# Kernel optimization log

Hardware: AMD Instinct MI355X
Metric: run time of the kernel (lower is better)

The kernel has to match this reference:

```python
import jax, jax.numpy as jnp
import numpy as np

B, S, E, H, D, L, V, O = 64, 512, 512, 8, 64, 4, 50000, 1000
KW, STRIDE = 5, 5
L_OUT = (S - KW) // STRIDE + 1  # 102


def setup_inputs() -> dict:
    key = jax.random.key(0)
    ks = jax.random.split(key, 20)
    sc = 0.02
    inp = {
        'tokens': jax.random.randint(ks[0], (B, S), 0, V, dtype=jnp.int32),
        'emb': jax.random.normal(ks[1], (V + 1, E), jnp.float32) * sc,
        'Wq': jax.random.normal(ks[2], (L, H, E, D), jnp.float32) * sc,
        'bq': jnp.zeros((L, H, D), jnp.float32),
        'Wk': jax.random.normal(ks[3], (L, H, E, D), jnp.float32) * sc,
        'bk': jnp.zeros((L, H, D), jnp.float32),
        'Wv': jax.random.normal(ks[4], (L, H, E, D), jnp.float32) * sc,
        'bv': jnp.zeros((L, H, D), jnp.float32),
        'Wo': jax.random.normal(ks[5], (L, H * D, E), jnp.float32) * sc,
        'bo': jnp.zeros((L, E), jnp.float32),
        'W1': jax.random.normal(ks[6], (L, E, 2 * E), jnp.float32) * sc,
        'b1': jnp.zeros((L, 2 * E), jnp.float32),
        'W2': jax.random.normal(ks[7], (L, 2 * E, E), jnp.float32) * sc,
        'b2': jnp.zeros((L, E), jnp.float32),
        'Wc': jax.random.normal(ks[8], (KW, E, 1), jnp.float32) * sc,
        'bc': jnp.zeros((1,), jnp.float32),
        'Wd': jax.random.normal(ks[9], (L_OUT, O), jnp.float32) * sc,
        'bd': jnp.zeros((O,), jnp.float32),
    }
    return inp


def _l2_normalize(x, eps=1e-12):
    # tf.math.l2_normalize: x / sqrt(max(sum(x^2), eps))
    sq = jnp.sum(x * x, axis=-1, keepdims=True)
    return x * jax.lax.rsqrt(jnp.maximum(sq, eps))


def _forward(tokens, emb, Wq, bq, Wk, bk, Wv, bv, Wo, bo, W1, b1, W2, b2, Wc, bc, Wd, bd):
    mask = jnp.sign(tokens).astype(jnp.float32)[..., None]  # [B,S,1]
    out = emb[tokens] * mask                                 # [B,S,E]
    scale = 1.0 / jnp.sqrt(jnp.float32(E))                   # note: scaled by EMBEDDING_DIM, as in source
    for i in range(L):
        # per-head QKV projections, batched over heads
        q = jnp.einsum('bse,hed->bhsd', out, Wq[i]) + bq[i][None, :, None, :]
        k = jnp.einsum('bse,hed->bhsd', out, Wk[i]) + bk[i][None, :, None, :]
        v = jnp.einsum('bse,hed->bhsd', out, Wv[i]) + bv[i][None, :, None, :]
        scores = jnp.einsum('bhsd,bhtd->bhst', q, k) * scale
        attn = jax.nn.softmax(scores, axis=-1)
        heads = jnp.einsum('bhst,bhtd->bhsd', attn, v)       # [B,H,S,D]
        cat = heads.transpose(0, 2, 1, 3).reshape(B, S, H * D)
        mh = cat @ Wo[i] + bo[i]
        out = _l2_normalize(out + mh)
        ff = jax.nn.relu(out @ W1[i] + b1[i]) @ W2[i] + b2[i]
        out = ff + out
    # Conv1D(1, 5, strides=5) then squeeze channel, Dense over seq-length axis, softmax
    conv = jax.lax.conv_general_dilated(
        out, Wc, window_strides=(STRIDE,), padding='VALID',
        dimension_numbers=('NWC', 'WIO', 'NWC')) + bc          # [B,L_OUT,1]
    pooled = jnp.squeeze(conv, axis=-1)                        # [B,L_OUT]
    logits = pooled @ Wd + bd                                  # [B,O]
    return jax.nn.softmax(logits, axis=-1)


def reference(tokens, emb, Wq, bq, Wk, bk, Wv, bv, Wo, bo, W1, b1, W2, b2, Wc, bc, Wd, bd):
    return _forward(tokens, emb, Wq, bq, Wk, bk, Wv, bv, Wo, bo, W1, b1, W2, b2, Wc, bc, Wd, bd)
```

## Files before the change

### kernel.cpp

```cpp
#include <hip/hip_runtime.h>
#include <cstddef>

constexpr int B_ = 64, S_ = 512, E_ = 512, H_ = 8, D_ = 64, L_ = 4, O_ = 1000;
constexpr int BS_ = B_ * S_;
constexpr int HD_ = H_ * D_;
constexpr int QS_ = 1536;
constexpr int LOUT_ = 102;
constexpr float SCALE_ = 0.04419417382415922f;

typedef __bf16 bf16x8 __attribute__((ext_vector_type(8)));
typedef __bf16 bf16x4 __attribute__((ext_vector_type(4)));
typedef __bf16 bf16x2 __attribute__((ext_vector_type(2)));
typedef float floatx4 __attribute__((ext_vector_type(4)));

__device__ inline void load16_lds(const __bf16* g, __bf16* l) {
  __builtin_amdgcn_global_load_lds(
      (const __attribute__((address_space(1))) void*)g,
      (__attribute__((address_space(3))) void*)l, 16, 0, 0);
}

__global__ __launch_bounds__(256) void transpose_bf16(
    const float* __restrict__ in, __bf16* __restrict__ out,
    int R, int C, int IZ, int OZL, int OZH) {
  __shared__ float t[32][33];
  int z = blockIdx.z;
  const float* inz = in + (size_t)z * IZ;
  __bf16* outz = out + (size_t)(z >> 3) * OZL + (size_t)(z & 7) * OZH;
  int c0 = blockIdx.x * 32, r0 = blockIdx.y * 32;
  int x = threadIdx.x, y = threadIdx.y;
#pragma unroll
  for (int j = 0; j < 32; j += 8) t[y + j][x] = inz[(size_t)(r0 + y + j) * C + c0 + x];
  __syncthreads();
#pragma unroll
  for (int j = 0; j < 32; j += 8)
    outz[(size_t)(c0 + y + j) * R + r0 + x] = (__bf16)t[x][y + j];
}

__global__ __launch_bounds__(256) void bias_concat(
    const float* __restrict__ bq, const float* __restrict__ bk,
    const float* __restrict__ bv, float* __restrict__ qkvb) {
  int idx = blockIdx.x * 256 + threadIdx.x;
  int l = idx / QS_, j = idx % QS_;
  float v;
  if (j < 512) v = bq[l * 512 + j];
  else if (j < 1024) v = bk[l * 512 + j - 512];
  else v = bv[l * 512 + j - 1024];
  qkvb[idx] = v;
}

__global__ __launch_bounds__(256) void embed_kernel(
    const int* __restrict__ tokens, const float* __restrict__ emb,
    float* __restrict__ X, __bf16* __restrict__ Ab) {
  int idx = blockIdx.x * 256 + threadIdx.x;
  int bs = idx >> 7;
  int e = (idx & 127) << 2;
  int tok = tokens[bs];
  float4 v;
  if (tok == 0) v = make_float4(0.f, 0.f, 0.f, 0.f);
  else v = *(const float4*)(emb + (size_t)tok * E_ + e);
  size_t off = (size_t)bs * E_ + e;
  *(float4*)(X + off) = v;
  bf16x4 b;
  b[0] = (__bf16)v.x; b[1] = (__bf16)v.y; b[2] = (__bf16)v.z; b[3] = (__bf16)v.w;
  *(bf16x4*)(Ab + off) = b;
}

template <int RELU, int RES, int OUTF, int OUTB, int SCQ, int KT>
__global__ __launch_bounds__(256) void gemm_bf16(
    const __bf16* __restrict__ A, const __bf16* __restrict__ Bt,
    const float* __restrict__ bias, const float* __restrict__ Rsd,
    float* __restrict__ Cf, __bf16* __restrict__ Cb, int N, int lda, int Nt) {
  __shared__ __align__(16) __bf16 smem[24576];
  int tid = threadIdx.x;
  int lane = tid & 63, w = tid >> 6;
  int Mt8 = (int)(gridDim.x / Nt) >> 3;
  int xcd = blockIdx.x & 7;
  int j = blockIdx.x >> 3;
  int rr = j % (2 * Nt), chunk = j / (2 * Nt);
  int mt = xcd * Mt8 + chunk * 2 + (rr & 1);
  int nt = rr >> 1;
  int m0 = mt * 128, n0 = nt * 128;
  int q4 = lane >> 4, a_ = lane & 15;
  const int ldb = KT * 32;
  int r0s = tid >> 2, q0s = (tid & 3) ^ ((r0s >> 1) & 3);
  int r1s = 64 + (tid >> 2), q1s = (tid & 3) ^ ((r1s >> 1) & 3);
  const __bf16* Ag = A + (size_t)m0 * lda;
  const __bf16* Bg = Bt + (size_t)n0 * ldb;

  floatx4 acc[4][4];
#pragma unroll
  for (int i = 0; i < 4; ++i)
#pragma unroll
    for (int jj = 0; jj < 4; ++jj) acc[i][jj] = (floatx4)(0.0f);

  auto STAGE = [&](int kt, int bs) {
    __bf16* Ad = smem + bs * 4096;
    __bf16* Bd = smem + 12288 + bs * 4096;
    int k0 = kt * 32;
    load16_lds(Ag + (size_t)r0s * lda + k0 + q0s * 8, Ad + tid * 8);
    load16_lds(Ag + (size_t)r1s * lda + k0 + q1s * 8, Ad + (256 + tid) * 8);
    load16_lds(Bg + (size_t)r0s * ldb + k0 + q0s * 8, Bd + tid * 8);
    load16_lds(Bg + (size_t)r1s * ldb + k0 + q1s * 8, Bd + (256 + tid) * 8);
  };

  STAGE(0, 0);
  if (KT > 1) STAGE(1, 1);
#pragma unroll
  for (int kt = 0; kt < KT; ++kt) {
    if (kt + 2 < KT) {
      STAGE(kt + 2, (kt + 2) % 3);
      asm volatile("s_waitcnt vmcnt(8)" ::: "memory");
    } else if (kt + 1 < KT) {
      asm volatile("s_waitcnt vmcnt(4)" ::: "memory");
    } else {
      asm volatile("s_waitcnt vmcnt(0)" ::: "memory");
    }
    __builtin_amdgcn_s_barrier();
    __builtin_amdgcn_sched_barrier(0);
    const __bf16* As = smem + (kt % 3) * 4096;
    const __bf16* Bs = smem + 12288 + (kt % 3) * 4096;
    bf16x8 af[4], bfr[4];
#pragma unroll
    for (int i = 0; i < 4; ++i) {
      int row = (w & 1) * 64 + i * 16 + a_;
      int pc = q4 ^ ((row >> 1) & 3);
      af[i] = *(const bf16x8*)&As[(row * 4 + pc) * 8];
    }
#pragma unroll
    for (int jc = 0; jc < 4; ++jc) {
      int row = (w >> 1) * 64 + jc * 16 + a_;
      int pc = q4 ^ ((row >> 1) & 3);
      bfr[jc] = *(const bf16x8*)&Bs[(row * 4 + pc) * 8];
    }
    __builtin_amdgcn_s_setprio(1);
#pragma unroll
    for (int i = 0; i < 4; ++i)
#pragma unroll
      for (int jc = 0; jc < 4; ++jc)
        acc[i][jc] = __builtin_amdgcn_mfma_f32_16x16x32_bf16(bfr[jc], af[i],
                                                             acc[i][jc], 0, 0, 0);
    __builtin_amdgcn_s_setprio(0);
    asm volatile("" ::: "memory");
    __builtin_amdgcn_s_barrier();
  }
#pragma unroll
  for (int i = 0; i < 4; ++i) {
    int ml = (w & 1) * 64 + i * 16 + a_;
    int m = m0 + ml;
#pragma unroll
    for (int jc = 0; jc < 4; ++jc) {
      int nl = (w >> 1) * 64 + jc * 16 + q4 * 4;
      int n = n0 + nl;
      float4 bi = *(const float4*)(bias + n);
      floatx4 v = acc[i][jc];
      v[0] += bi.x; v[1] += bi.y; v[2] += bi.z; v[3] += bi.w;
      if (SCQ) { if (n < 512) v *= SCALE_; }
      if (RES) {
        float4 rv = *(const float4*)(Rsd + (size_t)m * N + n);
        v[0] += rv.x; v[1] += rv.y; v[2] += rv.z; v[3] += rv.w;
      }
      if (RELU) {
#pragma unroll
        for (int r = 0; r < 4; ++r) v[r] = fmaxf(v[r], 0.f);
      }
      if (OUTF) {
        float4 o = make_float4(v[0], v[1], v[2], v[3]);
        *(float4*)(Cf + (size_t)m * N + n) = o;
      }
      if (OUTB) {
        bf16x4 ob;
#pragma unroll
        for (int r = 0; r < 4; ++r) ob[r] = (__bf16)v[r];
        *(bf16x4*)&smem[ml * 136 + nl] = ob;
      }
    }
  }
  if (OUTB) {
    __syncthreads();
#pragma unroll
    for (int it = 0; it < 8; ++it) {
      int cid = it * 256 + tid;
      int row = cid >> 4, c8 = cid & 15;
      bf16x8 val = *(const bf16x8*)&smem[row * 136 + c8 * 8];
      *(bf16x8*)(Cb + (size_t)(m0 + row) * N + n0 + c8 * 8) = val;
    }
  }
}

__global__ __launch_bounds__(256, 2) void attn_bf16(__bf16* __restrict__ QKV) {
  __shared__ __align__(16) __bf16 Qs[256 * 64];
  __shared__ __align__(16) __bf16 Ks[64 * 64];
  __shared__ __align__(16) __bf16 Vt[64 * 64];
  __shared__ __align__(16) __bf16 Ps[64 * 64];
  int tid = threadIdx.x, lane = tid & 63, w = tid >> 6;
  int q4 = lane >> 4, a_ = lane & 15;
  int bid = blockIdx.x;
  int xg = bid & 7, slot = bid >> 3;
  int b = (slot >> 4) * 8 + xg;
  int r_ = slot & 15;
  int h = r_ >> 1;
  int s0 = (r_ & 1) * 256;
  size_t rowbase = (size_t)b * S_ * QS_ + h * 64;
  __bf16* Qg = QKV + rowbase;
  const __bf16* Kg = QKV + rowbase + 512;
  const __bf16* Vg = QKV + rowbase + 1024;
#pragma unroll
  for (int j = 0; j < 8; ++j) {
    int ci = j * 256 + w * 64 + lane;
    int row = ci >> 3, c = ci & 7, q = c ^ (row & 7);
    load16_lds(Qg + (size_t)(s0 + row) * QS_ + q * 8, Qs + (j * 256 + w * 64) * 8);
  }
  float mrow[4], lrow[4];
  floatx4 accO[4][4];
#pragma unroll
  for (int cc = 0; cc < 4; ++cc) {
    mrow[cc] = -3.0e38f; lrow[cc] = 0.f;
#pragma unroll
    for (int jc = 0; jc < 4; ++jc) accO[cc][jc] = (floatx4)(0.0f);
  }

  for (int t0 = 0; t0 < S_; t0 += 64) {
#pragma unroll
    for (int j = 0; j < 2; ++j) {
      int ci = j * 256 + w * 64 + lane;
      int row = ci >> 3, c = ci & 7, q = c ^ (row & 7);
      load16_lds(Kg + (size_t)(t0 + row) * QS_ + q * 8, Ks + (j * 256 + w * 64) * 8);
    }
    {
      int tp = tid & 31, dg = tid >> 5;
      bf16x8 v0 = *(const bf16x8*)(Vg + (size_t)(t0 + 2 * tp) * QS_ + dg * 8);
      bf16x8 v1 = *(const bf16x8*)(Vg + (size_t)(t0 + 2 * tp + 1) * QS_ + dg * 8);
#pragma unroll
      for (int x = 0; x < 8; ++x) {
        int d = dg * 8 + x;
        bf16x2 p; p[0] = v0[x]; p[1] = v1[x];
        *(bf16x2*)&Vt[(d * 8 + ((tp >> 2) ^ (d & 7))) * 8 + (tp & 3) * 2] = p;
      }
    }
    __syncthreads();
    bf16x8 af[2][4], bv[2][4];
#pragma unroll
    for (int ks = 0; ks < 2; ++ks)
#pragma unroll
      for (int jc = 0; jc < 4; ++jc) {
        int row = jc * 16 + a_, q = ks * 4 + q4;
        af[ks][jc] = *(const bf16x8*)&Ks[(row * 8 + (q ^ (row & 7))) * 8];
        bv[ks][jc] = *(const bf16x8*)&Vt[(row * 8 + (q ^ (row & 7))) * 8];
      }
#pragma unroll
    for (int cc = 0; cc < 4; ++cc) {
      int sbase = (cc * 4 + w) * 16;
      floatx4 sc[4];
#pragma unroll
      for (int jc = 0; jc < 4; ++jc) sc[jc] = (floatx4)(0.0f);
#pragma unroll
      for (int ks = 0; ks < 2; ++ks) {
        int row = sbase + a_, q = ks * 4 + q4;
        bf16x8 bq = *(const bf16x8*)&Qs[(row * 8 + (q ^ (row & 7))) * 8];
#pragma unroll
        for (int jc = 0; jc < 4; ++jc)
          sc[jc] = __builtin_amdgcn_mfma_f32_16x16x32_bf16(af[ks][jc], bq,
                                                           sc[jc], 0, 0, 0);
      }
      float mx = sc[0][0];
#pragma unroll
      for (int jc = 0; jc < 4; ++jc)
#pragma unroll
        for (int r = 0; r < 4; ++r) mx = fmaxf(mx, sc[jc][r]);
      mx = fmaxf(mx, __shfl_xor(mx, 16));
      mx = fmaxf(mx, __shfl_xor(mx, 32));
      float mnew = fmaxf(mrow[cc], mx);
      float alpha = __expf(mrow[cc] - mnew);
      mrow[cc] = mnew;
      float ps = 0.f;
      int prow = w * 16 + a_;
#pragma unroll
      for (int jc = 0; jc < 4; ++jc) {
        bf16x4 pb;
#pragma unroll
        for (int r = 0; r < 4; ++r) {
          float p = __expf(sc[jc][r] - mnew);
          ps += p;
          pb[r] = (__bf16)p;
        }
        int pc = jc * 2 + (q4 >> 1);
        *(bf16x4*)&Ps[(prow * 8 + (pc ^ (prow & 7))) * 8 + (q4 & 1) * 4] = pb;
      }
      ps += __shfl_xor(ps, 16);
      ps += __shfl_xor(ps, 32);
      lrow[cc] = lrow[cc] * alpha + ps;
      float aal[4];
#pragma unroll
      for (int r = 0; r < 4; ++r) aal[r] = __shfl(alpha, q4 * 4 + r);
#pragma unroll
      for (int jc = 0; jc < 4; ++jc) {
        floatx4 t = accO[cc][jc];
#pragma unroll
        for (int r = 0; r < 4; ++r) t[r] *= aal[r];
        accO[cc][jc] = t;
      }
#pragma unroll
      for (int ks = 0; ks < 2; ++ks) {
        int q = ks * 4 + q4;
        bf16x8 ap = *(const bf16x8*)&Ps[(prow * 8 + (q ^ (prow & 7))) * 8];
#pragma unroll
        for (int jc = 0; jc < 4; ++jc)
          accO[cc][jc] = __builtin_amdgcn_mfma_f32_16x16x32_bf16(
              ap, bv[ks][jc], accO[cc][jc], 0, 0, 0);
      }
    }
    __syncthreads();
  }
#pragma unroll
  for (int cc = 0; cc < 4; ++cc) {
    float inv = 1.f / lrow[cc];
    float linv[4];
#pragma unroll
    for (int r = 0; r < 4; ++r) linv[r] = __shfl(inv, q4 * 4 + r);
    int srow = s0 + (cc * 4 + w) * 16 + q4 * 4;
#pragma unroll
    for (int r = 0; r < 4; ++r)
#pragma unroll
      for (int jc = 0; jc < 4; ++jc)
        Qg[(size_t)(srow + r) * QS_ + jc * 16 + a_] =
            (__bf16)(accO[cc][jc][r] * linv[r]);
  }
}

__global__ __launch_bounds__(256) void addnorm_kernel(
    float* __restrict__ X, const __bf16* __restrict__ MH, __bf16* __restrict__ Ab) {
  int row = blockIdx.x * 4 + (threadIdx.x >> 6);
  int ln = threadIdx.x & 63;
  size_t off = (size_t)row * E_ + ln * 8;
  float xv[8];
  *(float4*)&xv[0] = *(const float4*)(X + off);
  *(float4*)&xv[4] = *(const float4*)(X + off + 4);
  bf16x8 mh = *(const bf16x8*)(MH + off);
  float ss = 0.f;
#pragma unroll
  for (int j = 0; j < 8; ++j) {
    xv[j] += (float)mh[j];
    ss += xv[j] * xv[j];
  }
#pragma unroll
  for (int o = 1; o < 64; o <<= 1) ss += __shfl_xor(ss, o);
  float inv = rsqrtf(fmaxf(ss, 1e-12f));
  bf16x8 ob;
#pragma unroll
  for (int j = 0; j < 8; ++j) {
    xv[j] *= inv;
    ob[j] = (__bf16)xv[j];
  }
  *(float4*)(X + off) = *(float4*)&xv[0];
  *(float4*)(X + off + 4) = *(float4*)&xv[4];
  *(bf16x8*)(Ab + off) = ob;
}

__global__ __launch_bounds__(256) void conv_pool_kernel(
    const float* __restrict__ X, const float* __restrict__ Wc,
    const float* __restrict__ bc, float* __restrict__ pooled) {
  int wid = blockIdx.x * 4 + (threadIdx.x >> 6);
  int ln = threadIdx.x & 63;
  int b = wid / LOUT_, l = wid % LOUT_;
  const float* xr = X + (size_t)b * S_ * E_ + (size_t)l * 5 * E_;
  float v = 0.f;
#pragma unroll
  for (int j = 0; j < 10; ++j) {
    int i = (j * 64 + ln) * 4;
    float4 x4 = *(const float4*)(xr + i);
    float4 w4 = *(const float4*)(Wc + i);
    v += x4.x * w4.x + x4.y * w4.y + x4.z * w4.z + x4.w * w4.w;
  }
#pragma unroll
  for (int o = 32; o >= 1; o >>= 1) v += __shfl_down(v, o);
  if (ln == 0) pooled[b * LOUT_ + l] = v + bc[0];
}

__global__ __launch_bounds__(256) void dense_softmax_kernel(
    const float* __restrict__ pooled, const float* __restrict__ Wd,
    const float* __restrict__ bd, float* __restrict__ out) {
  __shared__ float pl[LOUT_];
  __shared__ float red[256];
  __shared__ float lg[O_];
  int b = blockIdx.x, tid = threadIdx.x;
  if (tid < LOUT_) pl[tid] = pooled[b * LOUT_ + tid];
  __syncthreads();
  for (int o = tid; o < O_; o += 256) {
    float acc = bd[o];
#pragma unroll 6
    for (int l = 0; l < LOUT_; ++l) acc += pl[l] * Wd[l * O_ + o];
    lg[o] = acc;
  }
  __syncthreads();
  float mx = -3.0e38f;
  for (int o = tid; o < O_; o += 256) mx = fmaxf(mx, lg[o]);
  red[tid] = mx;
  __syncthreads();
  for (int s2 = 128; s2 > 0; s2 >>= 1) {
    if (tid < s2) red[tid] = fmaxf(red[tid], red[tid + s2]);
    __syncthreads();
  }
  mx = red[0];
  __syncthreads();
  float se = 0.f;
  for (int o = tid; o < O_; o += 256) {
    float e = __expf(lg[o] - mx);
    lg[o] = e;
    se += e;
  }
  red[tid] = se;
  __syncthreads();
  for (int s2 = 128; s2 > 0; s2 >>= 1) {
    if (tid < s2) red[tid] += red[tid + s2];
    __syncthreads();
  }
  float inv = 1.f / red[0];
  for (int o = tid; o < O_; o += 256) out[(size_t)b * O_ + o] = lg[o] * inv;
}

extern "C" void kernel_launch(void* const* d_in, const int* in_sizes, int n_in,
                              void* d_out, int out_size, void* d_ws, size_t ws_size,
                              hipStream_t stream) {
  const int* tokens = (const int*)d_in[0];
  const float* emb = (const float*)d_in[1];
  const float* Wq = (const float*)d_in[2];
  const float* bq = (const float*)d_in[3];
  const float* Wk = (const float*)d_in[4];
  const float* bk = (const float*)d_in[5];
  const float* Wv = (const float*)d_in[6];
  const float* bv = (const float*)d_in[7];
  const float* Wo = (const float*)d_in[8];
  const float* bo = (const float*)d_in[9];
  const float* W1 = (const float*)d_in[10];
  const float* b1 = (const float*)d_in[11];
  const float* W2 = (const float*)d_in[12];
  const float* b2 = (const float*)d_in[13];
  const float* Wc = (const float*)d_in[14];
  const float* bc = (const float*)d_in[15];
  const float* Wd = (const float*)d_in[16];
  const float* bd = (const float*)d_in[17];
  float* out = (float*)d_out;

  char* ws = (char*)d_ws;
  float* X = (float*)ws;
  __bf16* Ab = (__bf16*)(ws + 67108864);
  __bf16* QKVb = (__bf16*)(ws + 100663296);
  __bf16* FF1b = QKVb;
  __bf16* MHb = (__bf16*)(ws + 201326592);
  __bf16* Wt = (__bf16*)(ws + 234881024);
  __bf16* Wt_qkv = Wt;
  __bf16* Wt_o = Wt + 3145728;
  __bf16* Wt_1 = Wt + 4194304;
  __bf16* Wt_2 = Wt + 6291456;
  float* qkvbias = (float*)(ws + 251658240);
  float* pooled = qkvbias + 6144;

  dim3 tb(32, 8);
  transpose_bf16<<<dim3(2, 16, 32), tb, 0, stream>>>(Wq, Wt_qkv + 0,      512, 64, 32768, 786432, 32768);
  transpose_bf16<<<dim3(2, 16, 32), tb, 0, stream>>>(Wk, Wt_qkv + 262144, 512, 64, 32768, 786432, 32768);
  transpose_bf16<<<dim3(2, 16, 32), tb, 0, stream>>>(Wv, Wt_qkv + 524288, 512, 64, 32768, 786432, 32768);
  transpose_bf16<<<dim3(16, 16, 4), tb, 0, stream>>>(Wo, Wt_o, 512, 512, 262144, 0, 262144);
  transpose_bf16<<<dim3(32, 16, 4), tb, 0, stream>>>(W1, Wt_1, 512, 1024, 524288, 0, 524288);
  transpose_bf16<<<dim3(16, 32, 4), tb, 0, stream>>>(W2, Wt_2, 1024, 512, 524288, 0, 524288);
  bias_concat<<<dim3(24), dim3(256), 0, stream>>>(bq, bk, bv, qkvbias);

  embed_kernel<<<dim3(BS_ * E_ / 4 / 256), dim3(256), 0, stream>>>(tokens, emb, X, Ab);

  dim3 blk(256);
  for (int i = 0; i < L_; ++i) {
    gemm_bf16<0, 0, 0, 1, 1, 16><<<dim3(256 * 12), blk, 0, stream>>>(
        Ab, Wt_qkv + (size_t)i * 786432, qkvbias + i * QS_, nullptr, nullptr,
        QKVb, QS_, 512, 12);
    attn_bf16<<<dim3(1024), blk, 0, stream>>>(QKVb);
    gemm_bf16<0, 0, 0, 1, 0, 16><<<dim3(256 * 4), blk, 0, stream>>>(
        QKVb, Wt_o + (size_t)i * 262144, bo + i * E_, nullptr, nullptr, MHb,
        512, QS_, 4);
    addnorm_kernel<<<dim3(BS_ / 4), blk, 0, stream>>>(X, MHb, Ab);
    gemm_bf16<1, 0, 0, 1, 0, 16><<<dim3(256 * 8), blk, 0, stream>>>(
        Ab, Wt_1 + (size_t)i * 524288, b1 + (size_t)i * 2 * E_, nullptr, nullptr,
        FF1b, 1024, 512, 8);
    gemm_bf16<0, 1, 1, 1, 0, 32><<<dim3(256 * 4), blk, 0, stream>>>(
        FF1b, Wt_2 + (size_t)i * 524288, b2 + (size_t)i * E_, X, X, Ab,
        512, 1024, 4);
  }
  conv_pool_kernel<<<dim3(BS_ * LOUT_ / S_ / 4), blk, 0, stream>>>(X, Wc, bc, pooled);
  dense_softmax_kernel<<<dim3(B_), blk, 0, stream>>>(pooled, Wd, bd, out);
}
```

Before: 1.406 ms.

## Enlarge GEMM tiles to 256x256 with 512-thread blocks and double buffering

Moves the bf16 GEMM from 128x128 tiles with 256 threads and a three-stage LDS pipeline to 256x256 tiles with 512 threads (8 waves, each computing 128x64) and a two-stage buffer. The larger tile raises arithmetic intensity and cuts global reloads of A and B. The epilogue becomes two passes through a swizzled LDS staging buffer. In exchange the grid shrinks by four (as few as 256 blocks on the O-proj and FF2 GEMMs), which can leave CUs underused. Each thread also holds more accumulators, pressuring registers, and prefetch depth drops from two stages to one.

```diff
diff --git a/kernel.cpp b/kernel.cpp
--- a/kernel.cpp
+++ b/kernel.cpp
@@ -65,124 +65,125 @@
   *(bf16x4*)(Ab + off) = b;
 }
 
+#define GFENCE asm volatile("" ::: "memory")
+#define GBAR  do { GFENCE; __builtin_amdgcn_s_barrier(); GFENCE; } while (0)
+
 template <int RELU, int RES, int OUTF, int OUTB, int SCQ, int KT>
-__global__ __launch_bounds__(256) void gemm_bf16(
+__global__ __launch_bounds__(512, 2) void gemm_bf16(
     const __bf16* __restrict__ A, const __bf16* __restrict__ Bt,
     const float* __restrict__ bias, const float* __restrict__ Rsd,
     float* __restrict__ Cf, __bf16* __restrict__ Cb, int N, int lda, int Nt) {
-  __shared__ __align__(16) __bf16 smem[24576];
+  __shared__ __align__(16) __bf16 smem[32768];
   int tid = threadIdx.x;
-  int lane = tid & 63, w = tid >> 6;
+  int lane = tid & 63, w8 = tid >> 6;
+  int wm = w8 & 1, wn = w8 >> 1;
+  int q4 = lane >> 4, a_ = lane & 15;
   int Mt8 = (int)(gridDim.x / Nt) >> 3;
   int xcd = blockIdx.x & 7;
   int j = blockIdx.x >> 3;
   int rr = j % (2 * Nt), chunk = j / (2 * Nt);
   int mt = xcd * Mt8 + chunk * 2 + (rr & 1);
   int nt = rr >> 1;
-  int m0 = mt * 128, n0 = nt * 128;
-  int q4 = lane >> 4, a_ = lane & 15;
+  int m0 = mt * 256, n0 = nt * 256;
   const int ldb = KT * 32;
-  int r0s = tid >> 2, q0s = (tid & 3) ^ ((r0s >> 1) & 3);
-  int r1s = 64 + (tid >> 2), q1s = (tid & 3) ^ ((r1s >> 1) & 3);
+  int ci0 = tid, ci1 = 512 + tid;
+  int r0s = ci0 >> 2, q0s = (ci0 & 3) ^ ((r0s >> 1) & 3);
+  int r1s = ci1 >> 2, q1s = (ci1 & 3) ^ ((r1s >> 1) & 3);
   const __bf16* Ag = A + (size_t)m0 * lda;
   const __bf16* Bg = Bt + (size_t)n0 * ldb;
 
-  floatx4 acc[4][4];
-#pragma unroll
-  for (int i = 0; i < 4; ++i)
+  floatx4 acc[8][4];
+#pragma unroll
+  for (int i = 0; i < 8; ++i)
 #pragma unroll
     for (int jj = 0; jj < 4; ++jj) acc[i][jj] = (floatx4)(0.0f);
 
-  auto STAGE = [&](int kt, int bs) {
-    __bf16* Ad = smem + bs * 4096;
-    __bf16* Bd = smem + 12288 + bs * 4096;
-    int k0 = kt * 32;
-    load16_lds(Ag + (size_t)r0s * lda + k0 + q0s * 8, Ad + tid * 8);
-    load16_lds(Ag + (size_t)r1s * lda + k0 + q1s * 8, Ad + (256 + tid) * 8);
-    load16_lds(Bg + (size_t)r0s * ldb + k0 + q0s * 8, Bd + tid * 8);
-    load16_lds(Bg + (size_t)r1s * ldb + k0 + q1s * 8, Bd + (256 + tid) * 8);
+  auto STAGE = [&](int t, int s) {
+    __bf16* Ad = smem + s * 8192;
+    __bf16* Bd = smem + 16384 + s * 8192;
+    int k0 = t * 32;
+    load16_lds(Ag + (size_t)r0s * lda + k0 + q0s * 8, Ad + ci0 * 8);
+    load16_lds(Ag + (size_t)r1s * lda + k0 + q1s * 8, Ad + ci1 * 8);
+    load16_lds(Bg + (size_t)r0s * ldb + k0 + q0s * 8, Bd + ci0 * 8);
+    load16_lds(Bg + (size_t)r1s * ldb + k0 + q1s * 8, Bd + ci1 * 8);
   };
 
   STAGE(0, 0);
-  if (KT > 1) STAGE(1, 1);
-#pragma unroll
-  for (int kt = 0; kt < KT; ++kt) {
-    if (kt + 2 < KT) {
-      STAGE(kt + 2, (kt + 2) % 3);
-      asm volatile("s_waitcnt vmcnt(8)" ::: "memory");
-    } else if (kt + 1 < KT) {
+  for (int t = 0; t < KT; ++t) {
+    if (t + 1 < KT) {
+      STAGE(t + 1, (t + 1) & 1);
       asm volatile("s_waitcnt vmcnt(4)" ::: "memory");
     } else {
       asm volatile("s_waitcnt vmcnt(0)" ::: "memory");
     }
-    __builtin_amdgcn_s_barrier();
-    __builtin_amdgcn_sched_barrier(0);
-    const __bf16* As = smem + (kt % 3) * 4096;
-    const __bf16* Bs = smem + 12288 + (kt % 3) * 4096;
-    bf16x8 af[4], bfr[4];
-#pragma unroll
-    for (int i = 0; i < 4; ++i) {
-      int row = (w & 1) * 64 + i * 16 + a_;
-      int pc = q4 ^ ((row >> 1) & 3);
-      af[i] = *(const bf16x8*)&As[(row * 4 + pc) * 8];
-    }
-#pragma unroll
-    for (int jc = 0; jc < 4; ++jc) {
-      int row = (w >> 1) * 64 + jc * 16 + a_;
-      int pc = q4 ^ ((row >> 1) & 3);
-      bfr[jc] = *(const bf16x8*)&Bs[(row * 4 + pc) * 8];
-    }
-    __builtin_amdgcn_s_setprio(1);
-#pragma unroll
-    for (int i = 0; i < 4; ++i)
-#pragma unroll
-      for (int jc = 0; jc < 4; ++jc)
-        acc[i][jc] = __builtin_amdgcn_mfma_f32_16x16x32_bf16(bfr[jc], af[i],
-                                                             acc[i][jc], 0, 0, 0);
-    __builtin_amdgcn_s_setprio(0);
-    asm volatile("" ::: "memory");
-    __builtin_amdgcn_s_barrier();
-  }
-#pragma unroll
-  for (int i = 0; i < 4; ++i) {
-    int ml = (w & 1) * 64 + i * 16 + a_;
-    int m = m0 + ml;
-#pragma unroll
-    for (int jc = 0; jc < 4; ++jc) {
-      int nl = (w >> 1) * 64 + jc * 16 + q4 * 4;
-      int n = n0 + nl;
-      float4 bi = *(const float4*)(bias + n);
-      floatx4 v = acc[i][jc];
-      v[0] += bi.x; v[1] += bi.y; v[2] += bi.z; v[3] += bi.w;
-      if (SCQ) { if (n < 512) v *= SCALE_; }
-      if (RES) {
-        float4 rv = *(const float4*)(Rsd + (size_t)m * N + n);
-        v[0] += rv.x; v[1] += rv.y; v[2] += rv.z; v[3] += rv.w;
-      }
-      if (RELU) {
-#pragma unroll
-        for (int r = 0; r < 4; ++r) v[r] = fmaxf(v[r], 0.f);
-      }
-      if (OUTF) {
-        float4 o = make_float4(v[0], v[1], v[2], v[3]);
-        *(float4*)(Cf + (size_t)m * N + n) = o;
-      }
-      if (OUTB) {
-        bf16x4 ob;
-#pragma unroll
-        for (int r = 0; r < 4; ++r) ob[r] = (__bf16)v[r];
-        *(bf16x4*)&smem[ml * 136 + nl] = ob;
-      }
-    }
-  }
-  if (OUTB) {
-    __syncthreads();
-#pragma unroll
-    for (int it = 0; it < 8; ++it) {
-      int cid = it * 256 + tid;
-      int row = cid >> 4, c8 = cid & 15;
-      bf16x8 val = *(const bf16x8*)&smem[row * 136 + c8 * 8];
-      *(bf16x8*)(Cb + (size_t)(m0 + row) * N + n0 + c8 * 8) = val;
+    GBAR;
+    const __bf16* As = smem + (t & 1) * 8192;
+    const __bf16* Bs = smem + 16384 + (t & 1) * 8192;
+    bf16x8 bfr[4];
+#pragma unroll
+    for (int nf = 0; nf < 4; ++nf) {
+      int r_ = wn * 64 + nf * 16 + a_;
+      bfr[nf] = *(const bf16x8*)&Bs[(r_ * 4 + (q4 ^ ((r_ >> 1) & 3))) * 8];
+    }
+#pragma unroll
+    for (int mf = 0; mf < 8; ++mf) {
+      int r_ = wm * 128 + mf * 16 + a_;
+      bf16x8 af = *(const bf16x8*)&As[(r_ * 4 + (q4 ^ ((r_ >> 1) & 3))) * 8];
+#pragma unroll
+      for (int nf = 0; nf < 4; ++nf)
+        acc[mf][nf] = __builtin_amdgcn_mfma_f32_16x16x32_bf16(bfr[nf], af,
+                                                              acc[mf][nf], 0, 0, 0);
+    }
+    GBAR;
+  }
+
+#pragma unroll 1
+  for (int pass = 0; pass < 2; ++pass) {
+    GBAR;
+    if (wm == pass) {
+#pragma unroll
+      for (int mf = 0; mf < 8; ++mf) {
+        int lr = mf * 16 + a_;
+        int m = m0 + pass * 128 + lr;
+#pragma unroll
+        for (int nf = 0; nf < 4; ++nf) {
+          int nl = wn * 64 + nf * 16 + q4 * 4;
+          int n = n0 + nl;
+          float4 bi = *(const float4*)(bias + n);
+          floatx4 v = acc[mf][nf];
+          v[0] += bi.x; v[1] += bi.y; v[2] += bi.z; v[3] += bi.w;
+          if (SCQ) { if (n < 512) v *= SCALE_; }
+          if (RES) {
+            float4 rv = *(const float4*)(Rsd + (size_t)m * N + n);
+            v[0] += rv.x; v[1] += rv.y; v[2] += rv.z; v[3] += rv.w;
+          }
+          if (RELU) {
+#pragma unroll
+            for (int r = 0; r < 4; ++r) v[r] = fmaxf(v[r], 0.f);
+          }
+          if (OUTF) {
+            float4 o = make_float4(v[0], v[1], v[2], v[3]);
+            *(float4*)(Cf + (size_t)m * N + n) = o;
+          }
+          if (OUTB) {
+            bf16x4 ob;
+#pragma unroll
+            for (int r = 0; r < 4; ++r) ob[r] = (__bf16)v[r];
+            int ch = nl >> 3;
+            *(bf16x4*)&smem[lr * 256 + (ch ^ (lr & 7)) * 8 + (q4 & 1) * 4] = ob;
+          }
+        }
+      }
+    }
+    GBAR;
+    if (OUTB) {
+#pragma unroll
+      for (int it = 0; it < 8; ++it) {
+        int cid = it * 512 + tid;
+        int row = cid >> 5, ch = cid & 31;
+        bf16x8 val = *(const bf16x8*)&smem[row * 256 + (ch ^ (row & 7)) * 8];
+        *(bf16x8*)(Cb + (size_t)(m0 + pass * 128 + row) * N + n0 + ch * 8) = val;
+      }
     }
   }
 }
@@ -467,21 +468,22 @@
   embed_kernel<<<dim3(BS_ * E_ / 4 / 256), dim3(256), 0, stream>>>(tokens, emb, X, Ab);
 
   dim3 blk(256);
+  dim3 blk512(512);
   for (int i = 0; i < L_; ++i) {
-    gemm_bf16<0, 0, 0, 1, 1, 16><<<dim3(256 * 12), blk, 0, stream>>>(
+    gemm_bf16<0, 0, 0, 1, 1, 16><<<dim3(768), blk512, 0, stream>>>(
         Ab, Wt_qkv + (size_t)i * 786432, qkvbias + i * QS_, nullptr, nullptr,
-        QKVb, QS_, 512, 12);
+        QKVb, QS_, 512, 6);
     attn_bf16<<<dim3(1024), blk, 0, stream>>>(QKVb);
-    gemm_bf16<0, 0, 0, 1, 0, 16><<<dim3(256 * 4), blk, 0, stream>>>(
+    gemm_bf16<0, 0, 0, 1, 0, 16><<<dim3(256), blk512, 0, stream>>>(
         QKVb, Wt_o + (size_t)i * 262144, bo + i * E_, nullptr, nullptr, MHb,
-        512, QS_, 4);
+        512, QS_, 2);
     addnorm_kernel<<<dim3(BS_ / 4), blk, 0, stream>>>(X, MHb, Ab);
-    gemm_bf16<1, 0, 0, 1, 0, 16><<<dim3(256 * 8), blk, 0, stream>>>(
+    gemm_bf16<1, 0, 0, 1, 0, 16><<<dim3(512), blk512, 0, stream>>>(
         Ab, Wt_1 + (size_t)i * 524288, b1 + (size_t)i * 2 * E_, nullptr, nullptr,
-        FF1b, 1024, 512, 8);
-    gemm_bf16<0, 1, 1, 1, 0, 32><<<dim3(256 * 4), blk, 0, stream>>>(
+        FF1b, 1024, 512, 4);
+    gemm_bf16<0, 1, 1, 1, 0, 32><<<dim3(256), blk512, 0, stream>>>(
         FF1b, Wt_2 + (size_t)i * 524288, b2 + (size_t)i * E_, X, X, Ab,
-        512, 1024, 4);
+        512, 1024, 2);
   }
   conv_pool_kernel<<<dim3(BS_ * LOUT_ / S_ / 4), blk, 0, stream>>>(X, Wc, bc, pooled);
   dense_softmax_kernel<<<dim3(B_), blk, 0, stream>>>(pooled, Wd, bd, out);
```

New measurement: 1.494 ms. 1.06x slower.
